# Kernel optimization log

Measured on AMD Instinct MI355X. Metric: run time of the kernel, lower is better.

Reference implementation:

```python
import jax, jax.numpy as jnp
import numpy as np

N = 100000
E = 1600000


def graph_conv(x, src, dst, W_rel, b_rel, W_root, n_nodes):
    # PyG GraphConv (aggr='add'): out = lin_rel(sum_j x_j) + lin_root(x)
    agg = jax.ops.segment_sum(x[src], dst, num_segments=n_nodes)  # [N, in]
    return agg @ W_rel + b_rel + x @ W_root


def _glorot(key, shape):
    fan_in = shape[0]
    return jax.random.normal(key, shape, dtype=jnp.float32) / jnp.sqrt(jnp.float32(fan_in))


def setup_inputs() -> dict:
    key = jax.random.key(0)
    ks = jax.random.split(key, 16)
    x = jax.random.normal(ks[0], (N, 48), dtype=jnp.float32)
    additional_x = jax.random.normal(ks[1], (N, 16), dtype=jnp.float32)
    lf_embedding = jax.random.normal(ks[2], (N, 16), dtype=jnp.float32)
    edge_index = jax.random.randint(ks[3], (2, E), 0, N, dtype=jnp.int64)
    # conv1: 64 -> 32 ; conv2: 48 -> 48 ; conv3: 48 -> 16
    return {
        "x": x,
        "edge_index": edge_index,
        "additional_x": additional_x,
        "lf_embedding": lf_embedding,
        "W1_rel": _glorot(ks[4], (64, 32)),
        "b1": jnp.zeros((32,), dtype=jnp.float32),
        "W1_root": _glorot(ks[5], (64, 32)),
        "W2_rel": _glorot(ks[6], (48, 48)),
        "b2": jnp.zeros((48,), dtype=jnp.float32),
        "W2_root": _glorot(ks[7], (48, 48)),
        "W3_rel": _glorot(ks[8], (48, 16)),
        "b3": jnp.zeros((16,), dtype=jnp.float32),
        "W3_root": _glorot(ks[9], (48, 16)),
    }


def reference(x, edge_index, additional_x, lf_embedding,
              W1_rel, b1, W1_root, W2_rel, b2, W2_root, W3_rel, b3, W3_root):
    src, dst = edge_index[0], edge_index[1]
    n = x.shape[0]
    h = jnp.concatenate([x, additional_x], axis=1)            # [N, 64]
    h = jax.nn.relu(graph_conv(h, src, dst, W1_rel, b1, W1_root, n))  # [N, 32]
    h = jnp.concatenate([h, lf_embedding], axis=1)            # [N, 48]
    h = jax.nn.relu(graph_conv(h, src, dst, W2_rel, b2, W2_root, n))  # [N, 48]
    h = graph_conv(h, src, dst, W3_rel, b3, W3_root, n)       # [N, 16]
    return h + additional_x
```

## Files before the change

kernel.cpp:

```cpp
#include <hip/hip_runtime.h>

#define NODES_MAX 100000
#define EDGES_MAX 1600000
#define BN 256
#define NBUCK ((NODES_MAX + BN - 1) / BN)
#define B_PART 256
#define SCAN_CHUNK 1024

__device__ float g_ws[(size_t)NODES_MAX * 160];
__device__ unsigned short g_tb[(size_t)NODES_MAX * 112];
__device__ int g_rowptr[NODES_MAX + 1];
__device__ int g_csr[EDGES_MAX];
__device__ unsigned g_be[EDGES_MAX];
__device__ int g_mat[NBUCK * B_PART];
__device__ int g_bsum[(NBUCK * B_PART + SCAN_CHUNK - 1) / SCAN_CHUNK + 1];

__device__ __forceinline__ unsigned short f2bf(float f) {
    union { float f; unsigned u; } c; c.f = f;
    unsigned r = (c.u + 0x7FFFu + ((c.u >> 16) & 1u)) >> 16;
    return (unsigned short)r;
}
__device__ __forceinline__ float bflo(unsigned u) {
    union { unsigned u; float f; } c; c.u = u << 16; return c.f;
}
__device__ __forceinline__ float bfhi(unsigned u) {
    union { unsigned u; float f; } c; c.u = u & 0xFFFF0000u; return c.f;
}

__global__ __launch_bounds__(1024) void k_bcount(const int* __restrict__ edge, int E,
                                                 int nbuck, int chunk) {
    __shared__ int h[NBUCK];
    for (int i = threadIdx.x; i < nbuck; i += 1024) h[i] = 0;
    __syncthreads();
    const int lo = blockIdx.x * chunk, hi = min(E, lo + chunk);
    for (int e = lo + threadIdx.x; e < hi; e += 1024)
        atomicAdd(&h[edge[E + e] >> 8], 1);
    __syncthreads();
    for (int k = threadIdx.x; k < nbuck; k += 1024)
        g_mat[k * B_PART + blockIdx.x] = h[k];
}

__global__ __launch_bounds__(256) void k_scan_local(int M) {
    __shared__ int ssum[256];
    const int tid = threadIdx.x;
    const int base = blockIdx.x * SCAN_CHUNK + tid * 4;
    int v0 = (base + 0 < M) ? g_mat[base + 0] : 0;
    int v1 = (base + 1 < M) ? g_mat[base + 1] : 0;
    int v2 = (base + 2 < M) ? g_mat[base + 2] : 0;
    int v3 = (base + 3 < M) ? g_mat[base + 3] : 0;
    int s = v0 + v1 + v2 + v3;
    ssum[tid] = s;
    __syncthreads();
    for (int off = 1; off < 256; off <<= 1) {
        int v = (tid >= off) ? ssum[tid - off] : 0;
        __syncthreads();
        ssum[tid] += v;
        __syncthreads();
    }
    int run = ssum[tid] - s;
    if (base + 0 < M) g_mat[base + 0] = run;
    run += v0;
    if (base + 1 < M) g_mat[base + 1] = run;
    run += v1;
    if (base + 2 < M) g_mat[base + 2] = run;
    run += v2;
    if (base + 3 < M) g_mat[base + 3] = run;
    if (tid == 255) g_bsum[blockIdx.x] = ssum[255];
}

__global__ __launch_bounds__(1024) void k_scan_bsums(int nb) {
    __shared__ int ssum[1024];
    const int tid = threadIdx.x;
    int s = (tid < nb) ? g_bsum[tid] : 0;
    ssum[tid] = s;
    __syncthreads();
    for (int off = 1; off < 1024; off <<= 1) {
        int v = (tid >= off) ? ssum[tid - off] : 0;
        __syncthreads();
        ssum[tid] += v;
        __syncthreads();
    }
    if (tid < nb) g_bsum[tid] = ssum[tid] - s;
}

__global__ __launch_bounds__(1024) void k_bpart(const int* __restrict__ edge, int E,
                                                int nbuck, int chunk) {
    __shared__ int cur[NBUCK];
    for (int k = threadIdx.x; k < nbuck; k += 1024) {
        int idx = k * B_PART + blockIdx.x;
        cur[k] = g_mat[idx] + g_bsum[idx >> 10];
    }
    __syncthreads();
    const int lo = blockIdx.x * chunk, hi = min(E, lo + chunk);
    for (int e = lo + threadIdx.x; e < hi; e += 1024) {
        int s = edge[e], d = edge[E + e];
        int pos = atomicAdd(&cur[d >> 8], 1);
        g_be[pos] = ((unsigned)s << 8) | (unsigned)(d & (BN - 1));
    }
}

__global__ __launch_bounds__(BN) void k_csr(int N, int E, int nbuck) {
    const int b = blockIdx.x;
    const int nlo = b * BN;
    const int ebase = g_mat[b * B_PART] + g_bsum[(b * B_PART) >> 10];
    const int eend = (b + 1 < nbuck)
        ? (g_mat[(b + 1) * B_PART] + g_bsum[((b + 1) * B_PART) >> 10]) : E;
    __shared__ int cnt[BN];
    __shared__ int pfx[BN];
    const int tid = threadIdx.x;
    cnt[tid] = 0;
    __syncthreads();
    for (int e = ebase + tid; e < eend; e += BN)
        atomicAdd(&cnt[g_be[e] & (BN - 1)], 1);
    __syncthreads();
    int v = cnt[tid];
    pfx[tid] = v;
    __syncthreads();
    for (int off = 1; off < BN; off <<= 1) {
        int t = (tid >= off) ? pfx[tid - off] : 0;
        __syncthreads();
        pfx[tid] += t;
        __syncthreads();
    }
    int excl = pfx[tid] - v;
    int n = nlo + tid;
    if (n < N) g_rowptr[n] = ebase + excl;
    if (b == 0 && tid == 0) g_rowptr[N] = E;
    cnt[tid] = excl;
    __syncthreads();
    for (int e = ebase + tid; e < eend; e += BN) {
        unsigned pv = g_be[e];
        int pos = atomicAdd(&cnt[pv & (BN - 1)], 1);
        g_csr[ebase + pos] = (int)(pv >> 8);
    }
}

template <int F, int RS>
__global__ __launch_bounds__(256) void k_gather_relu(size_t oTB, size_t oR, size_t oH, int N) {
    constexpr int L = F / 8;
    int tid = blockIdx.x * 256 + threadIdx.x;
    int node = tid / L, c = tid % L;
    if (node >= N) return;
    const unsigned short* __restrict__ tb = &g_tb[oTB];
    int j = g_rowptr[node];
    const int end = g_rowptr[node + 1];
    float s0 = 0.f, s1 = 0.f, s2 = 0.f, s3 = 0.f, s4 = 0.f, s5 = 0.f, s6 = 0.f, s7 = 0.f;
    for (; j + 3 < end; j += 4) {
        int sn0 = g_csr[j], sn1 = g_csr[j + 1], sn2 = g_csr[j + 2], sn3 = g_csr[j + 3];
        const uint4 v0 = *(const uint4*)&tb[(size_t)sn0 * RS + c * 8];
        const uint4 v1 = *(const uint4*)&tb[(size_t)sn1 * RS + c * 8];
        const uint4 v2 = *(const uint4*)&tb[(size_t)sn2 * RS + c * 8];
        const uint4 v3 = *(const uint4*)&tb[(size_t)sn3 * RS + c * 8];
        s0 += bflo(v0.x) + bflo(v1.x) + bflo(v2.x) + bflo(v3.x);
        s1 += bfhi(v0.x) + bfhi(v1.x) + bfhi(v2.x) + bfhi(v3.x);
        s2 += bflo(v0.y) + bflo(v1.y) + bflo(v2.y) + bflo(v3.y);
        s3 += bfhi(v0.y) + bfhi(v1.y) + bfhi(v2.y) + bfhi(v3.y);
        s4 += bflo(v0.z) + bflo(v1.z) + bflo(v2.z) + bflo(v3.z);
        s5 += bfhi(v0.z) + bfhi(v1.z) + bfhi(v2.z) + bfhi(v3.z);
        s6 += bflo(v0.w) + bflo(v1.w) + bflo(v2.w) + bflo(v3.w);
        s7 += bfhi(v0.w) + bfhi(v1.w) + bfhi(v2.w) + bfhi(v3.w);
    }
    for (; j < end; ++j) {
        int sn = g_csr[j];
        const uint4 v = *(const uint4*)&tb[(size_t)sn * RS + c * 8];
        s0 += bflo(v.x); s1 += bfhi(v.x);
        s2 += bflo(v.y); s3 += bfhi(v.y);
        s4 += bflo(v.z); s5 += bfhi(v.z);
        s6 += bflo(v.w); s7 += bfhi(v.w);
    }
    const size_t ro = oR + (size_t)node * F + c * 8;
    const float4 ra = *(const float4*)&g_ws[ro];
    const float4 rb = *(const float4*)&g_ws[ro + 4];
    float4 oa, ob;
    oa.x = fmaxf(s0 + ra.x, 0.f); oa.y = fmaxf(s1 + ra.y, 0.f);
    oa.z = fmaxf(s2 + ra.z, 0.f); oa.w = fmaxf(s3 + ra.w, 0.f);
    ob.x = fmaxf(s4 + rb.x, 0.f); ob.y = fmaxf(s5 + rb.y, 0.f);
    ob.z = fmaxf(s6 + rb.z, 0.f); ob.w = fmaxf(s7 + rb.w, 0.f);
    const size_t ho = oH + (size_t)node * F + c * 8;
    *(float4*)&g_ws[ho] = oa;
    *(float4*)&g_ws[ho + 4] = ob;
}

__global__ __launch_bounds__(256) void k_gather_out(size_t oTB, float* __restrict__ out, int N) {
    constexpr int F = 16, L = 2;
    int tid = blockIdx.x * 256 + threadIdx.x;
    int node = tid / L, c = tid % L;
    if (node >= N) return;
    const unsigned short* __restrict__ tb = &g_tb[oTB];
    int j = g_rowptr[node];
    const int end = g_rowptr[node + 1];
    float s0 = 0.f, s1 = 0.f, s2 = 0.f, s3 = 0.f, s4 = 0.f, s5 = 0.f, s6 = 0.f, s7 = 0.f;
    for (; j + 3 < end; j += 4) {
        int sn0 = g_csr[j], sn1 = g_csr[j + 1], sn2 = g_csr[j + 2], sn3 = g_csr[j + 3];
        const uint4 v0 = *(const uint4*)&tb[(size_t)sn0 * F + c * 8];
        const uint4 v1 = *(const uint4*)&tb[(size_t)sn1 * F + c * 8];
        const uint4 v2 = *(const uint4*)&tb[(size_t)sn2 * F + c * 8];
        const uint4 v3 = *(const uint4*)&tb[(size_t)sn3 * F + c * 8];
        s0 += bflo(v0.x) + bflo(v1.x) + bflo(v2.x) + bflo(v3.x);
        s1 += bfhi(v0.x) + bfhi(v1.x) + bfhi(v2.x) + bfhi(v3.x);
        s2 += bflo(v0.y) + bflo(v1.y) + bflo(v2.y) + bflo(v3.y);
        s3 += bfhi(v0.y) + bfhi(v1.y) + bfhi(v2.y) + bfhi(v3.y);
        s4 += bflo(v0.z) + bflo(v1.z) + bflo(v2.z) + bflo(v3.z);
        s5 += bfhi(v0.z) + bfhi(v1.z) + bfhi(v2.z) + bfhi(v3.z);
        s6 += bflo(v0.w) + bflo(v1.w) + bflo(v2.w) + bflo(v3.w);
        s7 += bfhi(v0.w) + bfhi(v1.w) + bfhi(v2.w) + bfhi(v3.w);
    }
    for (; j < end; ++j) {
        int sn = g_csr[j];
        const uint4 v = *(const uint4*)&tb[(size_t)sn * F + c * 8];
        s0 += bflo(v.x); s1 += bfhi(v.x);
        s2 += bflo(v.y); s3 += bfhi(v.y);
        s4 += bflo(v.z); s5 += bfhi(v.z);
        s6 += bflo(v.w); s7 += bfhi(v.w);
    }
    float* op = &out[(size_t)node * F + c * 8];
    float4 oa = *(float4*)op;
    float4 ob = *(float4*)(op + 4);
    oa.x += s0; oa.y += s1; oa.z += s2; oa.w += s3;
    ob.x += s4; ob.y += s5; ob.z += s6; ob.w += s7;
    *(float4*)op = oa;
    *(float4*)(op + 4) = ob;
}

#define L1_PADS 72
__global__ __launch_bounds__(512) void k_l1_transform(
        const float* __restrict__ x, const float* __restrict__ ax,
        const float* __restrict__ Wrel, const float* __restrict__ Wroot,
        const float* __restrict__ b, int N, size_t oTB1, size_t oR1) {
    __shared__ float sWrel[64 * 32];
    __shared__ float sWroot[64 * 32];
    __shared__ unsigned short sH[128 * L1_PADS];
    const int tid = threadIdx.x;
    if (tid < 512) {
        ((float4*)sWrel)[tid] = ((const float4*)Wrel)[tid];
        ((float4*)sWroot)[tid] = ((const float4*)Wroot)[tid];
    }
    const int n0 = blockIdx.x * 128;
    for (int i = tid; i < 128 * 16; i += 512) {
        int nl = i >> 4, g = i & 15, n = n0 + nl;
        float4 v = {0.f, 0.f, 0.f, 0.f};
        if (n < N) v = (g < 12) ? *(const float4*)&x[(size_t)n * 48 + g * 4]
                                : *(const float4*)&ax[(size_t)n * 16 + (g - 12) * 4];
        ushort4 hv;
        hv.x = f2bf(v.x); hv.y = f2bf(v.y); hv.z = f2bf(v.z); hv.w = f2bf(v.w);
        *(ushort4*)&sH[nl * L1_PADS + g * 4] = hv;
    }
    __syncthreads();
    const int jg = tid & 7, nlp = tid >> 3;
    const unsigned short* h0p = &sH[(nlp * 2 + 0) * L1_PADS];
    const unsigned short* h1p = &sH[(nlp * 2 + 1) * L1_PADS];
    float at[2][4] = {}, ar[2][4] = {};
    for (int k = 0; k < 64; ++k) {
        const float4 wr = *(const float4*)&sWrel[k * 32 + jg * 4];
        const float4 wo = *(const float4*)&sWroot[k * 32 + jg * 4];
        const float h0 = bflo(h0p[k]);
        const float h1 = bflo(h1p[k]);
        at[0][0] = fmaf(h0, wr.x, at[0][0]); at[0][1] = fmaf(h0, wr.y, at[0][1]);
        at[0][2] = fmaf(h0, wr.z, at[0][2]); at[0][3] = fmaf(h0, wr.w, at[0][3]);
        ar[0][0] = fmaf(h0, wo.x, ar[0][0]); ar[0][1] = fmaf(h0, wo.y, ar[0][1]);
        ar[0][2] = fmaf(h0, wo.z, ar[0][2]); ar[0][3] = fmaf(h0, wo.w, ar[0][3]);
        at[1][0] = fmaf(h1, wr.x, at[1][0]); at[1][1] = fmaf(h1, wr.y, at[1][1]);
        at[1][2] = fmaf(h1, wr.z, at[1][2]); at[1][3] = fmaf(h1, wr.w, at[1][3]);
        ar[1][0] = fmaf(h1, wo.x, ar[1][0]); ar[1][1] = fmaf(h1, wo.y, ar[1][1]);
        ar[1][2] = fmaf(h1, wo.z, ar[1][2]); ar[1][3] = fmaf(h1, wo.w, ar[1][3]);
    }
    const float4 bv = *(const float4*)&b[jg * 4];
    #pragma unroll
    for (int m = 0; m < 2; ++m) {
        int n = n0 + nlp * 2 + m;
        if (n < N) {
            ushort4 tv;
            tv.x = f2bf(at[m][0]); tv.y = f2bf(at[m][1]);
            tv.z = f2bf(at[m][2]); tv.w = f2bf(at[m][3]);
            *(ushort4*)&g_tb[oTB1 + (size_t)n * 32 + jg * 4] = tv;
            float4 rv;
            rv.x = ar[m][0] + bv.x; rv.y = ar[m][1] + bv.y;
            rv.z = ar[m][2] + bv.z; rv.w = ar[m][3] + bv.w;
            *(float4*)&g_ws[oR1 + (size_t)n * 32 + jg * 4] = rv;
        }
    }
}

#define L2_PAD 49
__global__ __launch_bounds__(384) void k_l2_transform(
        const float* __restrict__ lf,
        const float* __restrict__ Wrel, const float* __restrict__ Wroot,
        const float* __restrict__ b, int N,
        size_t oH1, size_t oTB2, size_t oR2) {
    __shared__ float sWrel[48 * 48];
    __shared__ float sWroot[48 * 48];
    __shared__ float sH[64 * L2_PAD];
    const int tid = threadIdx.x;
    for (int i = tid; i < 576; i += 384) {
        ((float4*)sWrel)[i] = ((const float4*)Wrel)[i];
        ((float4*)sWroot)[i] = ((const float4*)Wroot)[i];
    }
    const int n0 = blockIdx.x * 64;
    for (int i = tid; i < 64 * 48; i += 384) {
        int nl = i / 48, k = i % 48, n = n0 + nl;
        float v = 0.f;
        if (n < N) v = (k < 32) ? g_ws[oH1 + (size_t)n * 32 + k]
                                : lf[(size_t)n * 16 + (k - 32)];
        sH[nl * L2_PAD + k] = v;
    }
    __syncthreads();
    const int jg = tid % 12, nlp = tid / 12;
    const float* h0p = &sH[(nlp * 2 + 0) * L2_PAD];
    const float* h1p = &sH[(nlp * 2 + 1) * L2_PAD];
    float at[2][4] = {}, ar[2][4] = {};
    for (int k = 0; k < 48; ++k) {
        const float4 wr = *(const float4*)&sWrel[k * 48 + jg * 4];
        const float4 wo = *(const float4*)&sWroot[k * 48 + jg * 4];
        const float h0 = h0p[k];
        const float h1 = h1p[k];
        at[0][0] = fmaf(h0, wr.x, at[0][0]); at[0][1] = fmaf(h0, wr.y, at[0][1]);
        at[0][2] = fmaf(h0, wr.z, at[0][2]); at[0][3] = fmaf(h0, wr.w, at[0][3]);
        ar[0][0] = fmaf(h0, wo.x, ar[0][0]); ar[0][1] = fmaf(h0, wo.y, ar[0][1]);
        ar[0][2] = fmaf(h0, wo.z, ar[0][2]); ar[0][3] = fmaf(h0, wo.w, ar[0][3]);
        at[1][0] = fmaf(h1, wr.x, at[1][0]); at[1][1] = fmaf(h1, wr.y, at[1][1]);
        at[1][2] = fmaf(h1, wr.z, at[1][2]); at[1][3] = fmaf(h1, wr.w, at[1][3]);
        ar[1][0] = fmaf(h1, wo.x, ar[1][0]); ar[1][1] = fmaf(h1, wo.y, ar[1][1]);
        ar[1][2] = fmaf(h1, wo.z, ar[1][2]); ar[1][3] = fmaf(h1, wo.w, ar[1][3]);
    }
    const float4 bv = *(const float4*)&b[jg * 4];
    #pragma unroll
    for (int m = 0; m < 2; ++m) {
        int n = n0 + nlp * 2 + m;
        if (n < N) {
            ushort4 tv;
            tv.x = f2bf(at[m][0]); tv.y = f2bf(at[m][1]);
            tv.z = f2bf(at[m][2]); tv.w = f2bf(at[m][3]);
            *(ushort4*)&g_tb[oTB2 + (size_t)n * 64 + jg * 4] = tv;
            float4 rv;
            rv.x = ar[m][0] + bv.x; rv.y = ar[m][1] + bv.y;
            rv.z = ar[m][2] + bv.z; rv.w = ar[m][3] + bv.w;
            *(float4*)&g_ws[oR2 + (size_t)n * 48 + jg * 4] = rv;
        }
    }
}

#define L3_PAD 49
__global__ __launch_bounds__(256) void k_l3_transform(
        const float* __restrict__ ax,
        const float* __restrict__ Wrel, const float* __restrict__ Wroot,
        const float* __restrict__ b, int N,
        size_t oH2, size_t oTB3, float* __restrict__ out) {
    __shared__ float sWrel[48 * 16];
    __shared__ float sWroot[48 * 16];
    __shared__ float sH[128 * L3_PAD];
    const int tid = threadIdx.x;
    if (tid < 192) {
        ((float4*)sWrel)[tid] = ((const float4*)Wrel)[tid];
        ((float4*)sWroot)[tid] = ((const float4*)Wroot)[tid];
    }
    const int n0 = blockIdx.x * 128;
    for (int i = tid; i < 128 * 48; i += 256) {
        int nl = i / 48, k = i % 48, n = n0 + nl;
        sH[nl * L3_PAD + k] = (n < N) ? g_ws[oH2 + (size_t)n * 48 + k] : 0.f;
    }
    __syncthreads();
    const int jg = tid & 3, nlp = tid >> 2;
    const float* h0p = &sH[(nlp * 2 + 0) * L3_PAD];
    const float* h1p = &sH[(nlp * 2 + 1) * L3_PAD];
    float at[2][4] = {}, ar[2][4] = {};
    for (int k = 0; k < 48; ++k) {
        const float4 wr = *(const float4*)&sWrel[k * 16 + jg * 4];
        const float4 wo = *(const float4*)&sWroot[k * 16 + jg * 4];
        const float h0 = h0p[k];
        const float h1 = h1p[k];
        at[0][0] = fmaf(h0, wr.x, at[0][0]); at[0][1] = fmaf(h0, wr.y, at[0][1]);
        at[0][2] = fmaf(h0, wr.z, at[0][2]); at[0][3] = fmaf(h0, wr.w, at[0][3]);
        ar[0][0] = fmaf(h0, wo.x, ar[0][0]); ar[0][1] = fmaf(h0, wo.y, ar[0][1]);
        ar[0][2] = fmaf(h0, wo.z, ar[0][2]); ar[0][3] = fmaf(h0, wo.w, ar[0][3]);
        at[1][0] = fmaf(h1, wr.x, at[1][0]); at[1][1] = fmaf(h1, wr.y, at[1][1]);
        at[1][2] = fmaf(h1, wr.z, at[1][2]); at[1][3] = fmaf(h1, wr.w, at[1][3]);
        ar[1][0] = fmaf(h1, wo.x, ar[1][0]); ar[1][1] = fmaf(h1, wo.y, ar[1][1]);
        ar[1][2] = fmaf(h1, wo.z, ar[1][2]); ar[1][3] = fmaf(h1, wo.w, ar[1][3]);
    }
    const float4 bv = *(const float4*)&b[jg * 4];
    #pragma unroll
    for (int m = 0; m < 2; ++m) {
        int n = n0 + nlp * 2 + m;
        if (n < N) {
            ushort4 tv;
            tv.x = f2bf(at[m][0]); tv.y = f2bf(at[m][1]);
            tv.z = f2bf(at[m][2]); tv.w = f2bf(at[m][3]);
            *(ushort4*)&g_tb[oTB3 + (size_t)n * 16 + jg * 4] = tv;
            const float4 av = *(const float4*)&ax[(size_t)n * 16 + jg * 4];
            float4 rv;
            rv.x = ar[m][0] + bv.x + av.x; rv.y = ar[m][1] + bv.y + av.y;
            rv.z = ar[m][2] + bv.z + av.z; rv.w = ar[m][3] + bv.w + av.w;
            *(float4*)&out[(size_t)n * 16 + jg * 4] = rv;
        }
    }
}

extern "C" void kernel_launch(void* const* d_in, const int* in_sizes, int n_in,
                              void* d_out, int out_size, void* d_ws, size_t ws_size,
                              hipStream_t stream) {
    const float* x     = (const float*)d_in[0];
    const int*   edge  = (const int*)d_in[1];
    const float* ax    = (const float*)d_in[2];
    const float* lf    = (const float*)d_in[3];
    const float* W1rel = (const float*)d_in[4];
    const float* b1    = (const float*)d_in[5];
    const float* W1root= (const float*)d_in[6];
    const float* W2rel = (const float*)d_in[7];
    const float* b2    = (const float*)d_in[8];
    const float* W2root= (const float*)d_in[9];
    const float* W3rel = (const float*)d_in[10];
    const float* b3    = (const float*)d_in[11];
    const float* W3root= (const float*)d_in[12];
    float* out = (float*)d_out;

    const int N = in_sizes[0] / 48;
    const int E = in_sizes[1] / 2;
    const int nbuck = (N + BN - 1) / BN;
    const int chunk = (E + B_PART - 1) / B_PART;
    const int M = nbuck * B_PART;
    const int nb = (M + SCAN_CHUNK - 1) / SCAN_CHUNK;

    const size_t oR1 = 0;
    const size_t oH1 = (size_t)N * 32;
    const size_t oR2 = (size_t)N * 64;
    const size_t oH2 = (size_t)N * 112;
    const size_t oTB1 = 0;
    const size_t oTB2 = (size_t)N * 32;
    const size_t oTB3 = (size_t)N * 96;

    k_bcount<<<B_PART, 1024, 0, stream>>>(edge, E, nbuck, chunk);
    k_scan_local<<<nb, 256, 0, stream>>>(M);
    k_scan_bsums<<<1, 1024, 0, stream>>>(nb);
    k_bpart<<<B_PART, 1024, 0, stream>>>(edge, E, nbuck, chunk);
    k_csr<<<nbuck, BN, 0, stream>>>(N, E, nbuck);

    k_l1_transform<<<(N + 127) / 128, 512, 0, stream>>>(x, ax, W1rel, W1root, b1, N, oTB1, oR1);
    k_gather_relu<32, 32><<<(unsigned)(((size_t)N * 4 + 255) / 256), 256, 0, stream>>>(oTB1, oR1, oH1, N);
    k_l2_transform<<<(N + 63) / 64, 384, 0, stream>>>(lf, W2rel, W2root, b2, N, oH1, oTB2, oR2);
    k_gather_relu<48, 64><<<(unsigned)(((size_t)N * 6 + 255) / 256), 256, 0, stream>>>(oTB2, oR2, oH2, N);
    k_l3_transform<<<(N + 127) / 128, 256, 0, stream>>>(ax, W3rel, W3root, b3, N, oH2, oTB3, out);
    k_gather_out<<<(unsigned)(((size_t)N * 2 + 255) / 256), 256, 0, stream>>>(oTB3, out, N);
}
```

Before: 278.4 us.

## Pad CSR rows to multiples of four with dummy zero node for vectorized gathers

CSR construction is split into a counting pass, a scan over buckets and a fill pass. Each node's neighbour list is padded to a multiple of four, with the padding pointing at a dummy node N whose bf16 feature row is zeroed. The gather kernels then load four neighbour indices with a single int4 and drop the scalar tail loop. The cost is extra kernel launches in CSR build, about 1.5 padding entries per node on average (roughly 10% more edge reads), and a zero-row write in each transform kernel.

```diff
diff --git a/kernel.cpp b/kernel.cpp
--- a/kernel.cpp
+++ b/kernel.cpp
@@ -8,12 +8,13 @@
 #define SCAN_CHUNK 1024
 
 __device__ float g_ws[(size_t)NODES_MAX * 160];
-__device__ unsigned short g_tb[(size_t)NODES_MAX * 112];
+__device__ __attribute__((aligned(16))) unsigned short g_tb[(size_t)(NODES_MAX + 2) * 112];
 __device__ int g_rowptr[NODES_MAX + 1];
-__device__ int g_csr[EDGES_MAX];
+__device__ __attribute__((aligned(16))) int g_csr[EDGES_MAX + 3 * NODES_MAX + 16];
 __device__ unsigned g_be[EDGES_MAX];
 __device__ int g_mat[NBUCK * B_PART];
 __device__ int g_bsum[(NBUCK * B_PART + SCAN_CHUNK - 1) / SCAN_CHUNK + 1];
+__device__ int g_pb[NBUCK + 1];
 
 __device__ __forceinline__ unsigned short f2bf(float f) {
     union { float f; unsigned u; } c; c.f = f;
@@ -99,9 +100,8 @@
     }
 }
 
-__global__ __launch_bounds__(BN) void k_csr(int N, int E, int nbuck) {
+__global__ __launch_bounds__(BN) void k_csr_a(int N, int E, int nbuck) {
     const int b = blockIdx.x;
-    const int nlo = b * BN;
     const int ebase = g_mat[b * B_PART] + g_bsum[(b * B_PART) >> 10];
     const int eend = (b + 1 < nbuck)
         ? (g_mat[(b + 1) * B_PART] + g_bsum[((b + 1) * B_PART) >> 10]) : E;
@@ -113,8 +113,8 @@
     for (int e = ebase + tid; e < eend; e += BN)
         atomicAdd(&cnt[g_be[e] & (BN - 1)], 1);
     __syncthreads();
-    int v = cnt[tid];
-    pfx[tid] = v;
+    const int pdeg = (cnt[tid] + 3) & ~3;
+    pfx[tid] = pdeg;
     __syncthreads();
     for (int off = 1; off < BN; off <<= 1) {
         int t = (tid >= off) ? pfx[tid - off] : 0;
@@ -122,17 +122,49 @@
         pfx[tid] += t;
         __syncthreads();
     }
-    int excl = pfx[tid] - v;
-    int n = nlo + tid;
-    if (n < N) g_rowptr[n] = ebase + excl;
-    if (b == 0 && tid == 0) g_rowptr[N] = E;
-    cnt[tid] = excl;
+    const int n = b * BN + tid;
+    if (n < N) g_rowptr[n] = pfx[tid] - pdeg;
+    if (tid == BN - 1) g_pb[b] = pfx[BN - 1];
+}
+
+__global__ __launch_bounds__(512) void k_pscan(int nbuck, int N) {
+    __shared__ int s[512];
+    const int tid = threadIdx.x;
+    int v = (tid < nbuck) ? g_pb[tid] : 0;
+    s[tid] = v;
+    __syncthreads();
+    for (int off = 1; off < 512; off <<= 1) {
+        int t = (tid >= off) ? s[tid - off] : 0;
+        __syncthreads();
+        s[tid] += t;
+        __syncthreads();
+    }
+    if (tid < nbuck) g_pb[tid] = s[tid] - v;
+    if (tid == 511) g_rowptr[N] = s[511];
+}
+
+__global__ __launch_bounds__(BN) void k_csr_b(int N, int E, int nbuck) {
+    const int b = blockIdx.x;
+    const int ebase = g_mat[b * B_PART] + g_bsum[(b * B_PART) >> 10];
+    const int eend = (b + 1 < nbuck)
+        ? (g_mat[(b + 1) * B_PART] + g_bsum[((b + 1) * B_PART) >> 10]) : E;
+    __shared__ int cnt[BN];
+    const int tid = threadIdx.x;
+    const int base = g_pb[b];
+    const int n = b * BN + tid;
+    const int start = base + ((n < N) ? g_rowptr[n] : 0);
+    if (n < N) g_rowptr[n] = start;
+    cnt[tid] = start;
     __syncthreads();
     for (int e = ebase + tid; e < eend; e += BN) {
         unsigned pv = g_be[e];
         int pos = atomicAdd(&cnt[pv & (BN - 1)], 1);
-        g_csr[ebase + pos] = (int)(pv >> 8);
-    }
+        g_csr[pos] = (int)(pv >> 8);
+    }
+    __syncthreads();
+    const int endp = cnt[tid];
+    const int pend = start + ((endp - start + 3) & ~3);
+    for (int k = endp; k < pend; ++k) g_csr[k] = N;
 }
 
 template <int F, int RS>
@@ -145,12 +177,12 @@
     int j = g_rowptr[node];
     const int end = g_rowptr[node + 1];
     float s0 = 0.f, s1 = 0.f, s2 = 0.f, s3 = 0.f, s4 = 0.f, s5 = 0.f, s6 = 0.f, s7 = 0.f;
-    for (; j + 3 < end; j += 4) {
-        int sn0 = g_csr[j], sn1 = g_csr[j + 1], sn2 = g_csr[j + 2], sn3 = g_csr[j + 3];
-        const uint4 v0 = *(const uint4*)&tb[(size_t)sn0 * RS + c * 8];
-        const uint4 v1 = *(const uint4*)&tb[(size_t)sn1 * RS + c * 8];
-        const uint4 v2 = *(const uint4*)&tb[(size_t)sn2 * RS + c * 8];
-        const uint4 v3 = *(const uint4*)&tb[(size_t)sn3 * RS + c * 8];
+    for (; j < end; j += 4) {
+        const int4 sn = *(const int4*)&g_csr[j];
+        const uint4 v0 = *(const uint4*)&tb[(size_t)sn.x * RS + c * 8];
+        const uint4 v1 = *(const uint4*)&tb[(size_t)sn.y * RS + c * 8];
+        const uint4 v2 = *(const uint4*)&tb[(size_t)sn.z * RS + c * 8];
+        const uint4 v3 = *(const uint4*)&tb[(size_t)sn.w * RS + c * 8];
         s0 += bflo(v0.x) + bflo(v1.x) + bflo(v2.x) + bflo(v3.x);
         s1 += bfhi(v0.x) + bfhi(v1.x) + bfhi(v2.x) + bfhi(v3.x);
         s2 += bflo(v0.y) + bflo(v1.y) + bflo(v2.y) + bflo(v3.y);
@@ -159,14 +191,6 @@
         s5 += bfhi(v0.z) + bfhi(v1.z) + bfhi(v2.z) + bfhi(v3.z);
         s6 += bflo(v0.w) + bflo(v1.w) + bflo(v2.w) + bflo(v3.w);
         s7 += bfhi(v0.w) + bfhi(v1.w) + bfhi(v2.w) + bfhi(v3.w);
-    }
-    for (; j < end; ++j) {
-        int sn = g_csr[j];
-        const uint4 v = *(const uint4*)&tb[(size_t)sn * RS + c * 8];
-        s0 += bflo(v.x); s1 += bfhi(v.x);
-        s2 += bflo(v.y); s3 += bfhi(v.y);
-        s4 += bflo(v.z); s5 += bfhi(v.z);
-        s6 += bflo(v.w); s7 += bfhi(v.w);
     }
     const size_t ro = oR + (size_t)node * F + c * 8;
     const float4 ra = *(const float4*)&g_ws[ro];
@@ -190,12 +214,12 @@
     int j = g_rowptr[node];
     const int end = g_rowptr[node + 1];
     float s0 = 0.f, s1 = 0.f, s2 = 0.f, s3 = 0.f, s4 = 0.f, s5 = 0.f, s6 = 0.f, s7 = 0.f;
-    for (; j + 3 < end; j += 4) {
-        int sn0 = g_csr[j], sn1 = g_csr[j + 1], sn2 = g_csr[j + 2], sn3 = g_csr[j + 3];
-        const uint4 v0 = *(const uint4*)&tb[(size_t)sn0 * F + c * 8];
-        const uint4 v1 = *(const uint4*)&tb[(size_t)sn1 * F + c * 8];
-        const uint4 v2 = *(const uint4*)&tb[(size_t)sn2 * F + c * 8];
-        const uint4 v3 = *(const uint4*)&tb[(size_t)sn3 * F + c * 8];
+    for (; j < end; j += 4) {
+        const int4 sn = *(const int4*)&g_csr[j];
+        const uint4 v0 = *(const uint4*)&tb[(size_t)sn.x * F + c * 8];
+        const uint4 v1 = *(const uint4*)&tb[(size_t)sn.y * F + c * 8];
+        const uint4 v2 = *(const uint4*)&tb[(size_t)sn.z * F + c * 8];
+        const uint4 v3 = *(const uint4*)&tb[(size_t)sn.w * F + c * 8];
         s0 += bflo(v0.x) + bflo(v1.x) + bflo(v2.x) + bflo(v3.x);
         s1 += bfhi(v0.x) + bfhi(v1.x) + bfhi(v2.x) + bfhi(v3.x);
         s2 += bflo(v0.y) + bflo(v1.y) + bflo(v2.y) + bflo(v3.y);
@@ -205,14 +229,6 @@
         s6 += bflo(v0.w) + bflo(v1.w) + bflo(v2.w) + bflo(v3.w);
         s7 += bfhi(v0.w) + bfhi(v1.w) + bfhi(v2.w) + bfhi(v3.w);
     }
-    for (; j < end; ++j) {
-        int sn = g_csr[j];
-        const uint4 v = *(const uint4*)&tb[(size_t)sn * F + c * 8];
-        s0 += bflo(v.x); s1 += bfhi(v.x);
-        s2 += bflo(v.y); s3 += bfhi(v.y);
-        s4 += bflo(v.z); s5 += bfhi(v.z);
-        s6 += bflo(v.w); s7 += bfhi(v.w);
-    }
     float* op = &out[(size_t)node * F + c * 8];
     float4 oa = *(float4*)op;
     float4 ob = *(float4*)(op + 4);
@@ -231,6 +247,7 @@
     __shared__ float sWroot[64 * 32];
     __shared__ unsigned short sH[128 * L1_PADS];
     const int tid = threadIdx.x;
+    if (blockIdx.x == 0 && tid < 32) g_tb[oTB1 + (size_t)N * 32 + tid] = 0;
     if (tid < 512) {
         ((float4*)sWrel)[tid] = ((const float4*)Wrel)[tid];
         ((float4*)sWroot)[tid] = ((const float4*)Wroot)[tid];
@@ -291,6 +308,7 @@
     __shared__ float sWroot[48 * 48];
     __shared__ float sH[64 * L2_PAD];
     const int tid = threadIdx.x;
+    if (blockIdx.x == 0 && tid < 64) g_tb[oTB2 + (size_t)N * 64 + tid] = 0;
     for (int i = tid; i < 576; i += 384) {
         ((float4*)sWrel)[i] = ((const float4*)Wrel)[i];
         ((float4*)sWroot)[i] = ((const float4*)Wroot)[i];
@@ -349,6 +367,7 @@
     __shared__ float sWroot[48 * 16];
     __shared__ float sH[128 * L3_PAD];
     const int tid = threadIdx.x;
+    if (blockIdx.x == 0 && tid < 16) g_tb[oTB3 + (size_t)N * 16 + tid] = 0;
     if (tid < 192) {
         ((float4*)sWrel)[tid] = ((const float4*)Wrel)[tid];
         ((float4*)sWroot)[tid] = ((const float4*)Wroot)[tid];
@@ -425,14 +444,16 @@
     const size_t oR2 = (size_t)N * 64;
     const size_t oH2 = (size_t)N * 112;
     const size_t oTB1 = 0;
-    const size_t oTB2 = (size_t)N * 32;
-    const size_t oTB3 = (size_t)N * 96;
+    const size_t oTB2 = (((size_t)(N + 1) * 32) + 63) & ~(size_t)63;
+    const size_t oTB3 = oTB2 + (size_t)(N + 1) * 64;
 
     k_bcount<<<B_PART, 1024, 0, stream>>>(edge, E, nbuck, chunk);
     k_scan_local<<<nb, 256, 0, stream>>>(M);
     k_scan_bsums<<<1, 1024, 0, stream>>>(nb);
     k_bpart<<<B_PART, 1024, 0, stream>>>(edge, E, nbuck, chunk);
-    k_csr<<<nbuck, BN, 0, stream>>>(N, E, nbuck);
+    k_csr_a<<<nbuck, BN, 0, stream>>>(N, E, nbuck);
+    k_pscan<<<1, 512, 0, stream>>>(nbuck, N);
+    k_csr_b<<<nbuck, BN, 0, stream>>>(N, E, nbuck);
 
     k_l1_transform<<<(N + 127) / 128, 512, 0, stream>>>(x, ax, W1rel, W1root, b1, N, oTB1, oR1);
     k_gather_relu<32, 32><<<(unsigned)(((size_t)N * 4 + 255) / 256), 256, 0, stream>>>(oTB1, oR1, oH1, N);
```

Result: no change. 278.5 us (+0.0%).
